# Kernel optimization log

Hardware: AMD Instinct MI355X
Metric: run time of the kernel (lower is better)

The kernel has to match this reference:

```python
import jax, jax.numpy as jnp
import numpy as np

B, T, C = 2, 2048, 1024
NH, NKV, HD = 16, 4, 64
VEC = 32  # ve_gate_channels


def _rope(x, cos, sin):
    d = x.shape[-1] // 2
    x1, x2 = x[..., :d], x[..., d:]
    return jnp.concatenate([x1 * cos + x2 * sin, -x1 * sin + x2 * cos], axis=-1)


def _rmsnorm(x):
    eps = jnp.finfo(x.dtype).eps
    return x * jax.lax.rsqrt(jnp.mean(x * x, axis=-1, keepdims=True) + eps)


def setup_inputs() -> dict:
    key = jax.random.key(0)
    ks = jax.random.split(key, 9)
    s = 0.02
    return {
        "x": jax.random.normal(ks[0], (B, T, C), jnp.float32),
        "ve": jax.random.normal(ks[1], (B, T, NKV * HD), jnp.float32),
        "cos": jax.random.normal(ks[2], (1, T, 1, HD // 2), jnp.float32),
        "sin": jax.random.normal(ks[3], (1, T, 1, HD // 2), jnp.float32),
        "Wq": jax.random.normal(ks[4], (C, NH * HD), jnp.float32) * s,
        "Wk": jax.random.normal(ks[5], (C, NKV * HD), jnp.float32) * s,
        "Wv": jax.random.normal(ks[6], (C, NKV * HD), jnp.float32) * s,
        "Wproj": jax.random.normal(ks[7], (C, C), jnp.float32) * s,
        "Wgate": jax.random.normal(ks[8], (VEC, NKV), jnp.float32) * s,
        "window_size": 1024,
    }


def reference(x, ve, cos, sin, Wq, Wk, Wv, Wproj, Wgate, window_size):
    Bx, Tx, Cx = x.shape
    q = (x @ Wq).reshape(Bx, Tx, NH, HD)
    k = (x @ Wk).reshape(Bx, Tx, NKV, HD)
    v = (x @ Wv).reshape(Bx, Tx, NKV, HD)

    # value-embedding gate (has_ve True for this layer)
    gate = 2.0 * jax.nn.sigmoid(x[..., :VEC] @ Wgate)  # [B,T,NKV]
    v = v + gate[..., None] * ve.reshape(Bx, Tx, NKV, HD)

    q, k = _rope(q, cos, sin), _rope(k, cos, sin)
    q, k = _rmsnorm(q), _rmsnorm(k)

    q = q.transpose(0, 2, 1, 3)  # [B,NH,T,HD]
    k = k.transpose(0, 2, 1, 3)  # [B,NKV,T,HD]
    v = v.transpose(0, 2, 1, 3)

    # GQA: each KV head serves NH//NKV consecutive q heads
    g = NH // NKV
    k = jnp.repeat(k, g, axis=1)
    v = jnp.repeat(v, g, axis=1)

    row = jnp.arange(Tx)[:, None]
    col = jnp.arange(Tx)[None, :]
    mask = (col <= row) & (col >= row - window_size)  # causal sliding window

    scores = jnp.einsum("bhqd,bhkd->bhqk", q, k) / np.sqrt(HD).astype(np.float32)
    scores = jnp.where(mask[None, None], scores, jnp.finfo(scores.dtype).min)
    attn = jax.nn.softmax(scores, axis=-1)
    y = jnp.einsum("bhqk,bhkd->bhqd", attn, v)

    y = y.transpose(0, 2, 1, 3).reshape(Bx, Tx, Cx)
    return y @ Wproj
```

## Files before the change

kernel.cpp:

```cpp
#include <hip/hip_runtime.h>

typedef __bf16 bf16x8 __attribute__((ext_vector_type(8)));
typedef float f32x4 __attribute__((ext_vector_type(4)));

__device__ inline float tof(float v) { return v; }
__device__ inline float tof(__bf16 v) { return (float)v; }

__device__ inline bf16x8 load8(const __bf16* p) { return *(const bf16x8*)p; }
__device__ inline bf16x8 load8(const float* p) {
    const float4 a = *(const float4*)p;
    const float4 b = *(const float4*)(p + 4);
    bf16x8 r;
    r[0] = (__bf16)a.x; r[1] = (__bf16)a.y; r[2] = (__bf16)a.z; r[3] = (__bf16)a.w;
    r[4] = (__bf16)b.x; r[5] = (__bf16)b.y; r[6] = (__bf16)b.z; r[7] = (__bf16)b.w;
    return r;
}

__device__ __forceinline__ void cp16(__bf16* lds, const __bf16* g) {
    __builtin_amdgcn_global_load_lds((__attribute__((address_space(1))) void*)g,
                                     (__attribute__((address_space(3))) void*)lds,
                                     16, 0, 0);
}

__global__ void sniff_kernel(const unsigned short* __restrict__ xs, int* flag) {
    if (threadIdx.x != 0) return;
    int bad = 0;
    for (int i = 0; i < 512; ++i) {
        unsigned int f = ((unsigned int)xs[i]) << 16;
        float v = __uint_as_float(f);
        float a = fabsf(v);
        if (!(a <= 1e4f) || (a != 0.f && a < 1e-6f)) bad++;
    }
    *flag = (bad > 32) ? 1 : 0;
}

template <typename T>
__device__ __forceinline__ void prep_body(
    const T* __restrict__ x, const T* __restrict__ ve,
    const T* __restrict__ cosp, const T* __restrict__ sinp,
    const T* __restrict__ Wq, const T* __restrict__ Wk,
    const T* __restrict__ Wv, const T* __restrict__ Wp, const T* __restrict__ Wg,
    __bf16* __restrict__ xb, __bf16* __restrict__ veb,
    float* __restrict__ cosf_, float* __restrict__ sinf_,
    __bf16* __restrict__ WqT, __bf16* __restrict__ WkT,
    __bf16* __restrict__ WvT, __bf16* __restrict__ WpT,
    float* __restrict__ gate, __bf16* tile)
{
    const int b = blockIdx.x, tid = threadIdx.x;

    if (b < 2624) {
        int g = b * 256 + tid;
        if (g < 524288) {
            *(bf16x8*)(xb + (size_t)g * 8) = load8(x + (size_t)g * 8);
        } else if (g < 655360) {
            int gg = g - 524288;
            *(bf16x8*)(veb + (size_t)gg * 8) = load8(ve + (size_t)gg * 8);
        } else if (g < 663552) {
            int gg = g - 655360;
            const T* s = cosp + (size_t)gg * 8; float* d = cosf_ + (size_t)gg * 8;
#pragma unroll
            for (int j = 0; j < 8; ++j) d[j] = tof(s[j]);
        } else {
            int gg = g - 663552;
            const T* s = sinp + (size_t)gg * 8; float* d = sinf_ + (size_t)gg * 8;
#pragma unroll
            for (int j = 0; j < 8; ++j) d[j] = tof(s[j]);
        }
    } else if (b < 3264) {
        int idx = b - 2624;
        const T* src; __bf16* dst; int C;
        if (idx < 256)      { src = Wq; dst = WqT; C = 1024; }
        else if (idx < 320) { src = Wk; dst = WkT; C = 256;  idx -= 256; }
        else if (idx < 384) { src = Wv; dst = WvT; C = 256;  idx -= 320; }
        else                { src = Wp; dst = WpT; C = 1024; idx -= 384; }
        const int ctiles = C >> 6;
        const int r0 = (idx / ctiles) * 64, c0 = (idx % ctiles) * 64;
#pragma unroll
        for (int i = 0; i < 2; ++i) {
            int c = tid + i * 256, ir = c >> 3, ic = (c & 7) * 8;
            *(bf16x8*)(&tile[ir * 72 + ic]) = load8(src + (size_t)(r0 + ir) * C + c0 + ic);
        }
        __syncthreads();
#pragma unroll
        for (int i = 0; i < 2; ++i) {
            int c = tid + i * 256, orr = c >> 3, okc = (c & 7) * 8;
            bf16x8 v;
#pragma unroll
            for (int j = 0; j < 8; ++j) v[j] = tile[(okc + j) * 72 + orr];
            *(bf16x8*)(dst + (size_t)(c0 + orr) * 1024 + r0 + okc) = v;
        }
    } else {
        int r = (b - 3264) * 256 + tid;
        float z[4] = {0.f, 0.f, 0.f, 0.f};
        for (int j = 0; j < 32; ++j) {
            float xv = tof(x[(size_t)r * 1024 + j]);
#pragma unroll
            for (int h = 0; h < 4; ++h) z[h] += xv * tof(Wg[j * 4 + h]);
        }
#pragma unroll
        for (int h = 0; h < 4; ++h) gate[r * 4 + h] = 2.f / (1.f + __expf(-z[h]));
    }
}

__global__ __launch_bounds__(256) void prep_kernel(
    const void* x, const void* ve, const void* cosp, const void* sinp,
    const void* Wq, const void* Wk, const void* Wv, const void* Wp, const void* Wg,
    __bf16* xb, __bf16* veb, float* cosf_, float* sinf_,
    __bf16* WqT, __bf16* WkT, __bf16* WvT, __bf16* WpT,
    float* gate, const int* __restrict__ flag)
{
    __shared__ __bf16 tile[64 * 72];
    if (*flag) {
        prep_body<float>((const float*)x, (const float*)ve, (const float*)cosp,
                         (const float*)sinp, (const float*)Wq, (const float*)Wk,
                         (const float*)Wv, (const float*)Wp, (const float*)Wg,
                         xb, veb, cosf_, sinf_, WqT, WkT, WvT, WpT, gate, tile);
    } else {
        prep_body<__bf16>((const __bf16*)x, (const __bf16*)ve, (const __bf16*)cosp,
                          (const __bf16*)sinp, (const __bf16*)Wq, (const __bf16*)Wk,
                          (const __bf16*)Wv, (const __bf16*)Wp, (const __bf16*)Wg,
                          xb, veb, cosf_, sinf_, WqT, WkT, WvT, WpT, gate, tile);
    }
}

__global__ __launch_bounds__(256) void qkv_kernel(
    const __bf16* __restrict__ xb,
    const __bf16* __restrict__ WqT, const __bf16* __restrict__ WkT,
    const __bf16* __restrict__ WvT, const __bf16* __restrict__ veb,
    const float* __restrict__ cosf_, const float* __restrict__ sinf_,
    const float* __restrict__ gate,
    __bf16* __restrict__ qo, __bf16* __restrict__ ko, __bf16* __restrict__ vo)
{
    const int row0 = blockIdx.x * 128;
    const int cb = blockIdx.y;
    const __bf16* BT; int col0, h, mode;
    if (cb < 16)      { BT = WqT; col0 = cb * 64;        h = cb;      mode = 0; }
    else if (cb < 20) { BT = WkT; col0 = (cb - 16) * 64; h = cb - 16; mode = 1; }
    else              { BT = WvT; col0 = (cb - 20) * 64; h = cb - 20; mode = 2; }

    __shared__ __align__(16) __bf16 As[128 * 32];
    __shared__ __align__(16) __bf16 Bs[64 * 32];

    const int tid  = threadIdx.x;
    const int w    = tid >> 6;
    const int lane = tid & 63;
    const int quad = lane >> 4;
    const int l15  = lane & 15;
    const int wr   = w * 32;

    f32x4 acc[2][4];
#pragma unroll
    for (int mi = 0; mi < 2; ++mi)
#pragma unroll
        for (int nj = 0; nj < 4; ++nj) acc[mi][nj] = (f32x4){0.f, 0.f, 0.f, 0.f};

    for (int kk = 0; kk < 1024; kk += 32) {
#pragma unroll
        for (int i = 0; i < 2; ++i) {
            int c = i * 256 + (w << 6) + lane;
            int rr = c >> 2, kc = (c & 3) << 3;
            cp16(&As[c << 3], &xb[(size_t)(row0 + rr) * 1024 + kk + kc]);
        }
        {
            int c = (w << 6) + lane;
            int rr = c >> 2, kc = (c & 3) << 3;
            cp16(&Bs[c << 3], &BT[(size_t)(col0 + rr) * 1024 + kk + kc]);
        }
        __syncthreads();
        bf16x8 a[2], bfr[4];
#pragma unroll
        for (int mi = 0; mi < 2; ++mi) a[mi]  = *(const bf16x8*)(&As[(wr + mi * 16 + l15) * 32 + quad * 8]);
#pragma unroll
        for (int nj = 0; nj < 4; ++nj) bfr[nj] = *(const bf16x8*)(&Bs[(nj * 16 + l15) * 32 + quad * 8]);
#pragma unroll
        for (int mi = 0; mi < 2; ++mi)
#pragma unroll
            for (int nj = 0; nj < 4; ++nj)
                acc[mi][nj] = __builtin_amdgcn_mfma_f32_16x16x32_bf16(a[mi], bfr[nj], acc[mi][nj], 0, 0, 0);
        __syncthreads();
    }

    if (mode < 2) {
        __bf16* dst = (mode == 0) ? qo : ko;
        const int nh = (mode == 0) ? 16 : 4;
#pragma unroll
        for (int mi = 0; mi < 2; ++mi) {
#pragma unroll
            for (int r = 0; r < 4; ++r) {
                int row = row0 + wr + mi * 16 + quad * 4 + r;
                int b = row >> 11, t = row & 2047;
                float c0 = cosf_[t * 32 + l15];
                float c1 = cosf_[t * 32 + 16 + l15];
                float s0 = sinf_[t * 32 + l15];
                float s1 = sinf_[t * 32 + 16 + l15];
                float v0 =  c0 * acc[mi][0][r] + s0 * acc[mi][2][r];
                float v1 =  c1 * acc[mi][1][r] + s1 * acc[mi][3][r];
                float v2 = -s0 * acc[mi][0][r] + c0 * acc[mi][2][r];
                float v3 = -s1 * acc[mi][1][r] + c1 * acc[mi][3][r];
                float ss = v0 * v0 + v1 * v1 + v2 * v2 + v3 * v3;
                ss += __shfl_xor(ss, 1); ss += __shfl_xor(ss, 2);
                ss += __shfl_xor(ss, 4); ss += __shfl_xor(ss, 8);
                float sc = rsqrtf(ss * (1.f / 64.f) + 1.1920929e-7f);
                size_t base = (((size_t)b * nh + h) * 2048 + t) * 64;
                dst[base + 0 * 16 + l15] = (__bf16)(v0 * sc);
                dst[base + 1 * 16 + l15] = (__bf16)(v1 * sc);
                dst[base + 2 * 16 + l15] = (__bf16)(v2 * sc);
                dst[base + 3 * 16 + l15] = (__bf16)(v3 * sc);
            }
        }
    } else {
#pragma unroll
        for (int mi = 0; mi < 2; ++mi) {
#pragma unroll
            for (int r = 0; r < 4; ++r) {
                int row = row0 + wr + mi * 16 + quad * 4 + r;
                int b = row >> 11, t = row & 2047;
                float g = gate[row * 4 + h];
                size_t obase = (((size_t)b * 4 + h) * 2048 + t) * 64;
#pragma unroll
                for (int nj = 0; nj < 4; ++nj) {
                    float val = acc[mi][nj][r] + g * tof(veb[(size_t)row * 256 + h * 64 + nj * 16 + l15]);
                    vo[obase + nj * 16 + l15] = (__bf16)val;
                }
            }
        }
    }
}

__global__ __launch_bounds__(256) void attn_kernel(
    const __bf16* __restrict__ qg, const __bf16* __restrict__ kg,
    const __bf16* __restrict__ vg, __bf16* __restrict__ yo,
    const int* __restrict__ winp)
{
    const int q0 = blockIdx.x * 128;
    const int hh = blockIdx.y, b = blockIdx.z;
    const int kvh = hh >> 2;
    const int W = winp[0];

    const int tid  = threadIdx.x;
    const int w    = tid >> 6;
    const int lane = tid & 63;
    const int quad = lane >> 4;
    const int l15  = lane & 15;

    __shared__ __align__(16) __bf16 Ks[2][64 * 72];
    __shared__ __align__(16) __bf16 Vt[2][64 * 72];
    __shared__ __align__(16) __bf16 Ps[4][32 * 72];

    bf16x8 qf[2][2];
#pragma unroll
    for (int i = 0; i < 2; ++i) {
        size_t qb = (((size_t)b * 16 + hh) * 2048 + q0 + w * 32 + i * 16 + l15) * 64;
        qf[i][0] = *(const bf16x8*)(&qg[qb + quad * 8]);
        qf[i][1] = *(const bf16x8*)(&qg[qb + 32 + quad * 8]);
    }

    f32x4 oacc[2][4];
    float lsum[2][4];
#pragma unroll
    for (int i = 0; i < 2; ++i)
#pragma unroll
        for (int n = 0; n < 4; ++n) {
            oacc[i][n] = (f32x4){0.f, 0.f, 0.f, 0.f};
            lsum[i][n] = 0.f;
        }

    const int lo = q0 - W;
    const int kt_lo = lo > 0 ? (lo >> 6) : 0;
    const int kt_hi = (q0 + 127) >> 6;
    const size_t kbase = ((size_t)b * 4 + kvh) * 2048 * 64;

    {
        const int k0 = kt_lo * 64;
#pragma unroll
        for (int i = 0; i < 2; ++i) {
            int c = i * 256 + tid;
            int rk = c >> 3, dk = (c & 7) * 8;
            bf16x8 kv = *(const bf16x8*)(&kg[kbase + (size_t)(k0 + rk) * 64 + dk]);
            *(bf16x8*)(&Ks[0][rk * 72 + dk]) = kv;
            int rv = c & 63, dv = ((c >> 6) & 7) * 8;
            bf16x8 vv = *(const bf16x8*)(&vg[kbase + (size_t)(k0 + rv) * 64 + dv]);
#pragma unroll
            for (int j = 0; j < 8; ++j) Vt[0][(dv + j) * 72 + rv] = vv[j];
        }
    }
    __syncthreads();

    int cur = 0;
    for (int kt = kt_lo; kt <= kt_hi; ++kt) {
        const int k0 = kt * 64;
        const bool need_mask = (k0 + 63 > q0) || (q0 + 127 - k0 > W);
        const bool pf = (kt < kt_hi);
        bf16x8 pk[2], pv[2];
        if (pf) {
            const int k0n = k0 + 64;
#pragma unroll
            for (int i = 0; i < 2; ++i) {
                int c = i * 256 + tid;
                int rk = c >> 3, dk = (c & 7) * 8;
                pk[i] = *(const bf16x8*)(&kg[kbase + (size_t)(k0n + rk) * 64 + dk]);
                int rv = c & 63, dv = ((c >> 6) & 7) * 8;
                pv[i] = *(const bf16x8*)(&vg[kbase + (size_t)(k0n + rv) * 64 + dv]);
            }
        }

        f32x4 sacc[2][4];
#pragma unroll
        for (int i = 0; i < 2; ++i)
#pragma unroll
            for (int n = 0; n < 4; ++n) sacc[i][n] = (f32x4){0.f, 0.f, 0.f, 0.f};
        const __bf16* Kc = &Ks[cur][0];
#pragma unroll
        for (int n = 0; n < 4; ++n) {
            bf16x8 b0 = *(const bf16x8*)(&Kc[(n * 16 + l15) * 72 + quad * 8]);
            bf16x8 b1 = *(const bf16x8*)(&Kc[(n * 16 + l15) * 72 + 32 + quad * 8]);
#pragma unroll
            for (int i = 0; i < 2; ++i) {
                sacc[i][n] = __builtin_amdgcn_mfma_f32_16x16x32_bf16(qf[i][0], b0, sacc[i][n], 0, 0, 0);
                sacc[i][n] = __builtin_amdgcn_mfma_f32_16x16x32_bf16(qf[i][1], b1, sacc[i][n], 0, 0, 0);
            }
        }

#pragma unroll
        for (int i = 0; i < 2; ++i) {
#pragma unroll
            for (int r = 0; r < 4; ++r) {
                const int row_g = q0 + w * 32 + i * 16 + quad * 4 + r;
#pragma unroll
                for (int n = 0; n < 4; ++n) {
                    float p = exp2f(fmaf(sacc[i][n][r], 0.18033688f, -11.5415603f));
                    if (need_mask) {
                        int col_g = k0 + n * 16 + l15;
                        bool ok = (col_g <= row_g) && (row_g - col_g <= W);
                        p = ok ? p : 0.f;
                    }
                    lsum[i][r] += p;
                    Ps[w][(i * 16 + quad * 4 + r) * 72 + n * 16 + l15] = (__bf16)p;
                }
            }
        }
        asm volatile("s_waitcnt lgkmcnt(0)" ::: "memory");

        const __bf16* Vc = &Vt[cur][0];
#pragma unroll
        for (int ks = 0; ks < 2; ++ks) {
            bf16x8 pfr0 = *(const bf16x8*)(&Ps[w][l15 * 72 + ks * 32 + quad * 8]);
            bf16x8 pfr1 = *(const bf16x8*)(&Ps[w][(16 + l15) * 72 + ks * 32 + quad * 8]);
#pragma unroll
            for (int n = 0; n < 4; ++n) {
                bf16x8 bv = *(const bf16x8*)(&Vc[(n * 16 + l15) * 72 + ks * 32 + quad * 8]);
                oacc[0][n] = __builtin_amdgcn_mfma_f32_16x16x32_bf16(pfr0, bv, oacc[0][n], 0, 0, 0);
                oacc[1][n] = __builtin_amdgcn_mfma_f32_16x16x32_bf16(pfr1, bv, oacc[1][n], 0, 0, 0);
            }
        }

        if (pf) {
            const int nxt = cur ^ 1;
#pragma unroll
            for (int i = 0; i < 2; ++i) {
                int c = i * 256 + tid;
                int rk = c >> 3, dk = (c & 7) * 8;
                *(bf16x8*)(&Ks[nxt][rk * 72 + dk]) = pk[i];
                int rv = c & 63, dv = ((c >> 6) & 7) * 8;
#pragma unroll
                for (int j = 0; j < 8; ++j) Vt[nxt][(dv + j) * 72 + rv] = pv[i][j];
            }
            cur = nxt;
        }
        __syncthreads();
    }

#pragma unroll
    for (int i = 0; i < 2; ++i) {
#pragma unroll
        for (int r = 0; r < 4; ++r) {
            float l = lsum[i][r];
            l += __shfl_xor(l, 1); l += __shfl_xor(l, 2);
            l += __shfl_xor(l, 4); l += __shfl_xor(l, 8);
            float inv = 1.f / l;
            int t = q0 + w * 32 + i * 16 + quad * 4 + r;
            size_t base = ((size_t)(b * 2048 + t)) * 1024 + hh * 64;
#pragma unroll
            for (int n = 0; n < 4; ++n)
                yo[base + n * 16 + l15] = (__bf16)(oacc[i][n][r] * inv);
        }
    }
}

__global__ __launch_bounds__(256) void proj_kernel(
    const __bf16* __restrict__ y, const __bf16* __restrict__ WpT,
    void* __restrict__ outp, const int* __restrict__ flag)
{
    const int isf32 = *flag;
    const int row0 = blockIdx.x * 128;
    const int col0 = blockIdx.y * 64;
    __shared__ __align__(16) __bf16 As[128 * 32];
    __shared__ __align__(16) __bf16 Bs[64 * 32];

    const int tid  = threadIdx.x;
    const int w    = tid >> 6;
    const int lane = tid & 63;
    const int quad = lane >> 4;
    const int l15  = lane & 15;
    const int wr   = w * 32;

    f32x4 acc[2][4];
#pragma unroll
    for (int mi = 0; mi < 2; ++mi)
#pragma unroll
        for (int nj = 0; nj < 4; ++nj) acc[mi][nj] = (f32x4){0.f, 0.f, 0.f, 0.f};

    for (int kk = 0; kk < 1024; kk += 32) {
#pragma unroll
        for (int i = 0; i < 2; ++i) {
            int c = i * 256 + (w << 6) + lane;
            int rr = c >> 2, kc = (c & 3) << 3;
            cp16(&As[c << 3], &y[(size_t)(row0 + rr) * 1024 + kk + kc]);
        }
        {
            int c = (w << 6) + lane;
            int rr = c >> 2, kc = (c & 3) << 3;
            cp16(&Bs[c << 3], &WpT[(size_t)(col0 + rr) * 1024 + kk + kc]);
        }
        __syncthreads();
        bf16x8 a[2], bfr[4];
#pragma unroll
        for (int mi = 0; mi < 2; ++mi) a[mi]  = *(const bf16x8*)(&As[(wr + mi * 16 + l15) * 32 + quad * 8]);
#pragma unroll
        for (int nj = 0; nj < 4; ++nj) bfr[nj] = *(const bf16x8*)(&Bs[(nj * 16 + l15) * 32 + quad * 8]);
#pragma unroll
        for (int mi = 0; mi < 2; ++mi)
#pragma unroll
            for (int nj = 0; nj < 4; ++nj)
                acc[mi][nj] = __builtin_amdgcn_mfma_f32_16x16x32_bf16(a[mi], bfr[nj], acc[mi][nj], 0, 0, 0);
        __syncthreads();
    }

#pragma unroll
    for (int mi = 0; mi < 2; ++mi)
#pragma unroll
        for (int r = 0; r < 4; ++r) {
            int row = row0 + wr + mi * 16 + quad * 4 + r;
            if (isf32) {
                float* out = (float*)outp;
#pragma unroll
                for (int nj = 0; nj < 4; ++nj)
                    out[(size_t)row * 1024 + col0 + nj * 16 + l15] = acc[mi][nj][r];
            } else {
                __bf16* out = (__bf16*)outp;
#pragma unroll
                for (int nj = 0; nj < 4; ++nj)
                    out[(size_t)row * 1024 + col0 + nj * 16 + l15] = (__bf16)acc[mi][nj][r];
            }
        }
}

extern "C" void kernel_launch(void* const* d_in, const int* in_sizes, int n_in,
                              void* d_out, int out_size, void* d_ws, size_t ws_size,
                              hipStream_t stream) {
    const int* win = (const int*)d_in[9];

    char* p = (char*)d_ws;
    int*    flag = (int*)p;                    p += 256;
    __bf16* q_ws = (__bf16*)p;                 p += (size_t)4194304 * 2;
    __bf16* k_ws = (__bf16*)p;                 p += (size_t)1048576 * 2;
    __bf16* v_ws = (__bf16*)p;                 p += (size_t)1048576 * 2;
    __bf16* y_ws = (__bf16*)p;                 p += (size_t)4194304 * 2;
    __bf16* xb   = (__bf16*)p;                 p += (size_t)4194304 * 2;
    __bf16* veb  = (__bf16*)p;                 p += (size_t)1048576 * 2;
    __bf16* WqT  = (__bf16*)p;                 p += (size_t)1048576 * 2;
    __bf16* WkT  = (__bf16*)p;                 p += (size_t)262144 * 2;
    __bf16* WvT  = (__bf16*)p;                 p += (size_t)262144 * 2;
    __bf16* WpT  = (__bf16*)p;                 p += (size_t)1048576 * 2;
    float*  cosf_ = (float*)p;                 p += (size_t)65536 * 4;
    float*  sinf_ = (float*)p;                 p += (size_t)65536 * 4;
    float*  gate  = (float*)p;                 p += (size_t)16384 * 4;

    sniff_kernel<<<1, 64, 0, stream>>>((const unsigned short*)d_in[0], flag);

    prep_kernel<<<3280, 256, 0, stream>>>(
        d_in[0], d_in[1], d_in[2], d_in[3], d_in[4], d_in[5], d_in[6], d_in[7],
        d_in[8], xb, veb, cosf_, sinf_, WqT, WkT, WvT, WpT, gate, flag);

    qkv_kernel<<<dim3(32, 24), 256, 0, stream>>>(xb, WqT, WkT, WvT, veb,
                                                 cosf_, sinf_, gate, q_ws, k_ws, v_ws);

    attn_kernel<<<dim3(16, 16, 2), 256, 0, stream>>>(q_ws, k_ws, v_ws, y_ws, win);

    proj_kernel<<<dim3(32, 16), 256, 0, stream>>>(y_ws, WpT, d_out, flag);
}
```

Before: 213.2 us.

## Store V transposed and stage K/V via async global-to-LDS loads with XOR swizzle

The QKV kernel now writes V in a transposed [b,h,d,t] layout using packed 4-element stores. This lets the attention kernel stage both K and V tiles with direct global_load_lds copies instead of going through registers, and drops the scalar LDS transpose of V. The padded LDS tiles are replaced by XOR-swizzled unpadded tiles to avoid bank conflicts. The sniff kernel is also parallelised across a wavefront. The risks are the uncoalesced transposed V writes in the QKV kernel and the correctness of the async-copy ordering, since the barrier now has to cover the LDS DMA completing.

Result: faster. 195.5 us (-8.3%).

```diff
diff --git a/kernel.cpp b/kernel.cpp
--- a/kernel.cpp
+++ b/kernel.cpp
@@ -1,6 +1,7 @@
 #include <hip/hip_runtime.h>
 
 typedef __bf16 bf16x8 __attribute__((ext_vector_type(8)));
+typedef __bf16 bf16x4 __attribute__((ext_vector_type(4)));
 typedef float f32x4 __attribute__((ext_vector_type(4)));
 
 __device__ inline float tof(float v) { return v; }
@@ -23,15 +24,18 @@
 }
 
 __global__ void sniff_kernel(const unsigned short* __restrict__ xs, int* flag) {
-    if (threadIdx.x != 0) return;
+    int tid = threadIdx.x;
     int bad = 0;
-    for (int i = 0; i < 512; ++i) {
+    for (int i = tid; i < 512; i += 64) {
         unsigned int f = ((unsigned int)xs[i]) << 16;
         float v = __uint_as_float(f);
         float a = fabsf(v);
         if (!(a <= 1e4f) || (a != 0.f && a < 1e-6f)) bad++;
     }
-    *flag = (bad > 32) ? 1 : 0;
+    bad += __shfl_xor(bad, 1);  bad += __shfl_xor(bad, 2);
+    bad += __shfl_xor(bad, 4);  bad += __shfl_xor(bad, 8);
+    bad += __shfl_xor(bad, 16); bad += __shfl_xor(bad, 32);
+    if (tid == 0) *flag = (bad > 32) ? 1 : 0;
 }
 
 template <typename T>
@@ -129,7 +133,7 @@
     const __bf16* __restrict__ WvT, const __bf16* __restrict__ veb,
     const float* __restrict__ cosf_, const float* __restrict__ sinf_,
     const float* __restrict__ gate,
-    __bf16* __restrict__ qo, __bf16* __restrict__ ko, __bf16* __restrict__ vo)
+    __bf16* __restrict__ qo, __bf16* __restrict__ ko, __bf16* __restrict__ vTo)
 {
     const int row0 = blockIdx.x * 128;
     const int cb = blockIdx.y;
@@ -211,17 +215,21 @@
     } else {
 #pragma unroll
         for (int mi = 0; mi < 2; ++mi) {
-#pragma unroll
-            for (int r = 0; r < 4; ++r) {
-                int row = row0 + wr + mi * 16 + quad * 4 + r;
-                int b = row >> 11, t = row & 2047;
-                float g = gate[row * 4 + h];
-                size_t obase = (((size_t)b * 4 + h) * 2048 + t) * 64;
-#pragma unroll
-                for (int nj = 0; nj < 4; ++nj) {
-                    float val = acc[mi][nj][r] + g * tof(veb[(size_t)row * 256 + h * 64 + nj * 16 + l15]);
-                    vo[obase + nj * 16 + l15] = (__bf16)val;
+            int rowb = row0 + wr + mi * 16 + quad * 4;
+            int b = rowb >> 11, t0 = rowb & 2047;
+#pragma unroll
+            for (int nj = 0; nj < 4; ++nj) {
+                int d = nj * 16 + l15;
+                bf16x4 pack;
+#pragma unroll
+                for (int r = 0; r < 4; ++r) {
+                    int row = rowb + r;
+                    float g = gate[row * 4 + h];
+                    float val = acc[mi][nj][r] + g * tof(veb[(size_t)row * 256 + h * 64 + d]);
+                    pack[r] = (__bf16)val;
                 }
+                size_t a = (((size_t)b * 4 + h) * 64 + d) * 2048 + t0;
+                *(bf16x4*)(&vTo[a]) = pack;
             }
         }
     }
@@ -229,7 +237,7 @@
 
 __global__ __launch_bounds__(256) void attn_kernel(
     const __bf16* __restrict__ qg, const __bf16* __restrict__ kg,
-    const __bf16* __restrict__ vg, __bf16* __restrict__ yo,
+    const __bf16* __restrict__ vTg, __bf16* __restrict__ yo,
     const int* __restrict__ winp)
 {
     const int q0 = blockIdx.x * 128;
@@ -243,8 +251,8 @@
     const int quad = lane >> 4;
     const int l15  = lane & 15;
 
-    __shared__ __align__(16) __bf16 Ks[2][64 * 72];
-    __shared__ __align__(16) __bf16 Vt[2][64 * 72];
+    __shared__ __align__(16) __bf16 Ks[2][64 * 64];
+    __shared__ __align__(16) __bf16 Vt[2][64 * 64];
     __shared__ __align__(16) __bf16 Ps[4][32 * 72];
 
     bf16x8 qf[2][2];
@@ -268,41 +276,27 @@
     const int lo = q0 - W;
     const int kt_lo = lo > 0 ? (lo >> 6) : 0;
     const int kt_hi = (q0 + 127) >> 6;
-    const size_t kbase = ((size_t)b * 4 + kvh) * 2048 * 64;
-
-    {
-        const int k0 = kt_lo * 64;
+    const size_t kvbase = ((size_t)b * 4 + kvh) * 2048 * 64;
+
+    auto stage = [&](int buf, int k0) {
 #pragma unroll
         for (int i = 0; i < 2; ++i) {
             int c = i * 256 + tid;
-            int rk = c >> 3, dk = (c & 7) * 8;
-            bf16x8 kv = *(const bf16x8*)(&kg[kbase + (size_t)(k0 + rk) * 64 + dk]);
-            *(bf16x8*)(&Ks[0][rk * 72 + dk]) = kv;
-            int rv = c & 63, dv = ((c >> 6) & 7) * 8;
-            bf16x8 vv = *(const bf16x8*)(&vg[kbase + (size_t)(k0 + rv) * 64 + dv]);
-#pragma unroll
-            for (int j = 0; j < 8; ++j) Vt[0][(dv + j) * 72 + rv] = vv[j];
-        }
-    }
+            int rr = c >> 3;
+            int jj = (c & 7) ^ (rr & 7);
+            cp16(&Ks[buf][c * 8], &kg[kvbase + (size_t)(k0 + rr) * 64 + jj * 8]);
+            cp16(&Vt[buf][c * 8], &vTg[kvbase + (size_t)rr * 2048 + k0 + jj * 8]);
+        }
+    };
+
+    stage(0, kt_lo * 64);
     __syncthreads();
 
     int cur = 0;
     for (int kt = kt_lo; kt <= kt_hi; ++kt) {
         const int k0 = kt * 64;
         const bool need_mask = (k0 + 63 > q0) || (q0 + 127 - k0 > W);
-        const bool pf = (kt < kt_hi);
-        bf16x8 pk[2], pv[2];
-        if (pf) {
-            const int k0n = k0 + 64;
-#pragma unroll
-            for (int i = 0; i < 2; ++i) {
-                int c = i * 256 + tid;
-                int rk = c >> 3, dk = (c & 7) * 8;
-                pk[i] = *(const bf16x8*)(&kg[kbase + (size_t)(k0n + rk) * 64 + dk]);
-                int rv = c & 63, dv = ((c >> 6) & 7) * 8;
-                pv[i] = *(const bf16x8*)(&vg[kbase + (size_t)(k0n + rv) * 64 + dv]);
-            }
-        }
+        if (kt < kt_hi) stage(cur ^ 1, k0 + 64);
 
         f32x4 sacc[2][4];
 #pragma unroll
@@ -312,8 +306,9 @@
         const __bf16* Kc = &Ks[cur][0];
 #pragma unroll
         for (int n = 0; n < 4; ++n) {
-            bf16x8 b0 = *(const bf16x8*)(&Kc[(n * 16 + l15) * 72 + quad * 8]);
-            bf16x8 b1 = *(const bf16x8*)(&Kc[(n * 16 + l15) * 72 + 32 + quad * 8]);
+            int m = n * 16 + l15;
+            bf16x8 b0 = *(const bf16x8*)(&Kc[m * 64 + (quad ^ (m & 7)) * 8]);
+            bf16x8 b1 = *(const bf16x8*)(&Kc[m * 64 + ((4 + quad) ^ (m & 7)) * 8]);
 #pragma unroll
             for (int i = 0; i < 2; ++i) {
                 sacc[i][n] = __builtin_amdgcn_mfma_f32_16x16x32_bf16(qf[i][0], b0, sacc[i][n], 0, 0, 0);
@@ -348,26 +343,15 @@
             bf16x8 pfr1 = *(const bf16x8*)(&Ps[w][(16 + l15) * 72 + ks * 32 + quad * 8]);
 #pragma unroll
             for (int n = 0; n < 4; ++n) {
-                bf16x8 bv = *(const bf16x8*)(&Vc[(n * 16 + l15) * 72 + ks * 32 + quad * 8]);
+                int m = n * 16 + l15;
+                bf16x8 bv = *(const bf16x8*)(&Vc[m * 64 + ((ks * 4 + quad) ^ (m & 7)) * 8]);
                 oacc[0][n] = __builtin_amdgcn_mfma_f32_16x16x32_bf16(pfr0, bv, oacc[0][n], 0, 0, 0);
                 oacc[1][n] = __builtin_amdgcn_mfma_f32_16x16x32_bf16(pfr1, bv, oacc[1][n], 0, 0, 0);
             }
         }
 
-        if (pf) {
-            const int nxt = cur ^ 1;
-#pragma unroll
-            for (int i = 0; i < 2; ++i) {
-                int c = i * 256 + tid;
-                int rk = c >> 3, dk = (c & 7) * 8;
-                *(bf16x8*)(&Ks[nxt][rk * 72 + dk]) = pk[i];
-                int rv = c & 63, dv = ((c >> 6) & 7) * 8;
-#pragma unroll
-                for (int j = 0; j < 8; ++j) Vt[nxt][(dv + j) * 72 + rv] = pv[i][j];
-            }
-            cur = nxt;
-        }
-        __syncthreads();
+        __syncthreads();
+        cur ^= 1;
     }
 
 #pragma unroll
@@ -464,7 +448,7 @@
     int*    flag = (int*)p;                    p += 256;
     __bf16* q_ws = (__bf16*)p;                 p += (size_t)4194304 * 2;
     __bf16* k_ws = (__bf16*)p;                 p += (size_t)1048576 * 2;
-    __bf16* v_ws = (__bf16*)p;                 p += (size_t)1048576 * 2;
+    __bf16* vT_ws= (__bf16*)p;                 p += (size_t)1048576 * 2;
     __bf16* y_ws = (__bf16*)p;                 p += (size_t)4194304 * 2;
     __bf16* xb   = (__bf16*)p;                 p += (size_t)4194304 * 2;
     __bf16* veb  = (__bf16*)p;                 p += (size_t)1048576 * 2;
@@ -483,9 +467,9 @@
         d_in[8], xb, veb, cosf_, sinf_, WqT, WkT, WvT, WpT, gate, flag);
 
     qkv_kernel<<<dim3(32, 24), 256, 0, stream>>>(xb, WqT, WkT, WvT, veb,
-                                                 cosf_, sinf_, gate, q_ws, k_ws, v_ws);
-
-    attn_kernel<<<dim3(16, 16, 2), 256, 0, stream>>>(q_ws, k_ws, v_ws, y_ws, win);
+                                                 cosf_, sinf_, gate, q_ws, k_ws, vT_ws);
+
+    attn_kernel<<<dim3(16, 16, 2), 256, 0, stream>>>(q_ws, k_ws, vT_ws, y_ws, win);
 
     proj_kernel<<<dim3(32, 16), 256, 0, stream>>>(y_ws, WpT, d_out, flag);
 }
```
